# Performance work log

Measured on AMD Instinct MI355X. Metric: run time of the kernel, lower is better.

The kernel has to match this reference:

```python
import jax, jax.numpy as jnp
import numpy as np

B, S, D = 2, 2048, 1024
H, KS, VS = 16, 64, 64

def setup_inputs() -> dict:
    key = jax.random.key(0)
    ks = jax.random.split(key, 11)
    s = 1.0 / np.sqrt(D)
    return {
        "query": jax.random.normal(ks[0], (B, S, D), jnp.float32),
        "key":   jax.random.normal(ks[1], (B, S, D), jnp.float32),
        "value": jax.random.normal(ks[2], (B, S, D), jnp.float32),
        # weights stored [in, out] (transpose of torch Linear)
        "Wq": jax.random.normal(ks[3], (D, H * KS), jnp.float32) * s,
        "bq": jnp.zeros((H * KS,), jnp.float32),
        "Wk": jax.random.normal(ks[4], (D, H * KS), jnp.float32) * s,
        "bk": jnp.zeros((H * KS,), jnp.float32),
        "Wv": jax.random.normal(ks[5], (D, H * VS), jnp.float32) * s,
        "bv": jnp.zeros((H * VS,), jnp.float32),
        "Wo": jax.random.normal(ks[6], (H * VS, D), jnp.float32) * s,
        "bo": jnp.zeros((D,), jnp.float32),
    }

def reference(query, key, value, Wq, bq, Wk, bk, Wv, bv, Wo, bo):
    b = query.shape[0]
    # projections + split heads -> [B, H, S, d]
    Q = (query @ Wq + bq).reshape(b, -1, H, KS).transpose(0, 2, 1, 3)
    K = (key   @ Wk + bk).reshape(b, -1, H, KS).transpose(0, 2, 1, 3)
    V = (value @ Wv + bv).reshape(b, -1, H, VS).transpose(0, 2, 1, 3)
    scores = jnp.einsum('bhqd,bhkd->bhqk', Q, K) / jnp.sqrt(jnp.float32(KS))
    attn = jax.nn.softmax(scores, axis=-1)  # dropout_rate=0.0 -> identity
    ctx = jnp.einsum('bhqk,bhkd->bhqd', attn, V)  # [B,H,S,VS]
    ctx = ctx.transpose(0, 2, 1, 3).reshape(b, attn.shape[-1], H * VS)
    out = ctx @ Wo + bo
    return out, attn
```

## Files before the change

kernel.cpp:

```cpp
#include <hip/hip_runtime.h>
#include <stdint.h>


typedef _Float16 f16;
typedef f16 f16x4 __attribute__((ext_vector_type(4)));
typedef f16 f16x8 __attribute__((ext_vector_type(8)));
typedef float f32x4 __attribute__((ext_vector_type(4)));
typedef uint32_t u32;
typedef u32 u32x4 __attribute__((ext_vector_type(4)));

#define L2E 1.4426950408889634f

__device__ __forceinline__ void gload16(const void* g, void* l) {
    __builtin_amdgcn_global_load_lds((__attribute__((address_space(1))) void*)g,
                                     (__attribute__((address_space(3))) void*)l,
                                     16, 0, 0);
}

__global__ __launch_bounds__(256) void k_cvt(const float* __restrict__ q,
                                             const float* __restrict__ k,
                                             const float* __restrict__ v,
                                             f16* __restrict__ dst)
{
    int z = blockIdx.z;
    const float* s = (z == 0) ? q : (z == 1) ? k : v;
    size_t i = (size_t)blockIdx.x * 256 + threadIdx.x;
    float4 f = ((const float4*)s)[i];
    f16x4 o = {(f16)f.x, (f16)f.y, (f16)f.z, (f16)f.w};
    *(f16x4*)(dst + (size_t)z * 4194304 + i * 4) = o;
}

__global__ __launch_bounds__(256) void k_wtrans(const float* __restrict__ w0,
                                                const float* __restrict__ w1,
                                                const float* __restrict__ w2,
                                                const float* __restrict__ w3,
                                                f16* __restrict__ wt)
{
    __shared__ f16 t[64][72];
    int z = blockIdx.z;
    const float* W = (z == 0) ? w0 : (z == 1) ? w1 : (z == 2) ? w2 : w3;
    f16* outp = wt + (size_t)z * 1048576;
    int tx = blockIdx.x, ty = blockIdx.y, tid = threadIdx.x;
#pragma unroll
    for (int r4 = 0; r4 < 4; r4++) {
        int row = r4 * 16 + (tid >> 4);
        int col = (tid & 15) * 4;
        float4 f = *(const float4*)(W + (size_t)(ty * 64 + row) * 1024 + tx * 64 + col);
        t[col + 0][row] = (f16)f.x; t[col + 1][row] = (f16)f.y;
        t[col + 2][row] = (f16)f.z; t[col + 3][row] = (f16)f.w;
    }
    __syncthreads();
#pragma unroll
    for (int cc = 0; cc < 2; cc++) {
        int c = tid + cc * 256;
        int row = c >> 3, ch = c & 7;
        f16x8 vv;
#pragma unroll
        for (int j = 0; j < 8; j++) vv[j] = t[row][ch * 8 + j];
        *(f16x8*)(outp + (size_t)(tx * 64 + row) * 1024 + ty * 64 + ch * 8) = vv;
    }
}

__global__ __launch_bounds__(256) void k_gemm(const f16* __restrict__ Ab,
                                              const f16* __restrict__ Wtb,
                                              const float* __restrict__ b0,
                                              const float* __restrict__ b1,
                                              const float* __restrict__ b2,
                                              void* __restrict__ o0,
                                              void* __restrict__ o1,
                                              int proj)
{
    __shared__ __align__(16) char As[16384];
    __shared__ __align__(16) char Bs[16384];
    const int tid = threadIdx.x;
    const int wv = tid >> 6, ln = tid & 63, lg = ln >> 4, li = ln & 15;
    const int m0 = blockIdx.y * 128, n0 = blockIdx.x * 128;
    const int wm = (wv >> 1) * 64, wn = (wv & 1) * 64;

    const f16* A; const f16* Bt; const float* bias; int mode;
    if (proj) {
        int z = blockIdx.z;
        A = Ab + (size_t)z * 4194304;
        Bt = Wtb + (size_t)z * 1048576;
        bias = (z == 0) ? b0 : (z == 1) ? b1 : b2;
        mode = (z == 2) ? 1 : 0;
    } else { A = Ab; Bt = Wtb; bias = b0; mode = 2; }

    const char* gA[4]; const char* gB[4];
#pragma unroll
    for (int c = 0; c < 4; c++) {
        int r = (wv * 4 + c) * 8 + (ln >> 3);
        int j = (ln & 7) ^ (r & 7);
        gA[c] = (const char*)A  + (size_t)(m0 + r) * 2048 + j * 16;
        gB[c] = (const char*)Bt + (size_t)(n0 + r) * 2048 + j * 16;
    }

    f32x4 acc[4][4] = {};
    for (int kt = 0; kt < 16; kt++) {
        __syncthreads();
#pragma unroll
        for (int c = 0; c < 4; c++) {
            gload16(gA[c] + kt * 128, As + (wv * 4 + c) * 1024);
            gload16(gB[c] + kt * 128, Bs + (wv * 4 + c) * 1024);
        }
        __syncthreads();
#pragma unroll
        for (int kk = 0; kk < 2; kk++) {
            f16x8 af[4], bf[4];
#pragma unroll
            for (int mi = 0; mi < 4; mi++) {
                int row = wm + mi * 16 + li;
                af[mi] = *(const f16x8*)(As + row * 128 + (((kk * 4 + lg) ^ (row & 7)) * 16));
            }
#pragma unroll
            for (int ni = 0; ni < 4; ni++) {
                int row = wn + ni * 16 + li;
                bf[ni] = *(const f16x8*)(Bs + row * 128 + (((kk * 4 + lg) ^ (row & 7)) * 16));
            }
#pragma unroll
            for (int mi = 0; mi < 4; mi++)
#pragma unroll
                for (int ni = 0; ni < 4; ni++)
                    acc[mi][ni] = __builtin_amdgcn_mfma_f32_16x16x32_f16(af[mi], bf[ni], acc[mi][ni], 0, 0, 0);
        }
    }

    float bvs[4];
#pragma unroll
    for (int ni = 0; ni < 4; ni++) bvs[ni] = bias[n0 + wn + ni * 16 + li];

    if (mode == 2) {
        float* O = (float*)o0;
#pragma unroll
        for (int mi = 0; mi < 4; mi++)
#pragma unroll
            for (int ni = 0; ni < 4; ni++) {
                int n = n0 + wn + ni * 16 + li;
#pragma unroll
                for (int r = 0; r < 4; r++) {
                    int m = m0 + wm + mi * 16 + lg * 4 + r;
                    O[(size_t)m * 1024 + n] = acc[mi][ni][r] + bvs[ni];
                }
            }
    } else if (mode == 0) {
        f16* O = (f16*)o0 + (size_t)blockIdx.z * 4194304;
#pragma unroll
        for (int mi = 0; mi < 4; mi++)
#pragma unroll
            for (int ni = 0; ni < 4; ni++) {
                int n = n0 + wn + ni * 16 + li;
                int h = n >> 6, d = n & 63;
#pragma unroll
                for (int r = 0; r < 4; r++) {
                    int m = m0 + wm + mi * 16 + lg * 4 + r;
                    int b = m >> 11, s = m & 2047;
                    O[(((size_t)b * 16 + h) * 2048 + s) * 64 + d] = (f16)(acc[mi][ni][r] + bvs[ni]);
                }
            }
    } else {
        f16* O = (f16*)o1;
#pragma unroll
        for (int mi = 0; mi < 4; mi++)
#pragma unroll
            for (int ni = 0; ni < 4; ni++) {
                int n = n0 + wn + ni * 16 + li;
                int h = n >> 6, d = n & 63;
                int mb = m0 + wm + mi * 16 + lg * 4;
                int b = mb >> 11, s = mb & 2047;
                f16x4 pk;
#pragma unroll
                for (int r = 0; r < 4; r++) pk[r] = (f16)(acc[mi][ni][r] + bvs[ni]);
                *(f16x4*)(O + (((size_t)b * 16 + h) * 64 + d) * 2048 + s) = pk;
            }
    }
}

__global__ __launch_bounds__(256) void k_attn(const f16* __restrict__ Qb,
                                              const f16* __restrict__ Kb,
                                              const f16* __restrict__ Vt,
                                              float* __restrict__ attn,
                                              f16* __restrict__ ctx)
{
    __shared__ __align__(16) char Ks[8192];
    __shared__ __align__(16) char Vs[8192];
    __shared__ __align__(16) char Ps[4][2048];
    const int tid = threadIdx.x, wv = tid >> 6, ln = tid & 63, lg = ln >> 4, li = ln & 15;
    const int bh = blockIdx.y;
    const int q0 = blockIdx.x * 64 + wv * 16;

    const f16* qrow = Qb + ((size_t)bh * 2048 + q0 + li) * 64 + lg * 8;
    f16x8 aq0 = *(const f16x8*)(qrow);
    f16x8 aq1 = *(const f16x8*)(qrow + 32);
#pragma unroll
    for (int j = 0; j < 8; j++) {
        aq0[j] = (f16)((float)aq0[j] * 0.125f);
        aq1[j] = (f16)((float)aq1[j] * 0.125f);
    }

    const int r0 = tid >> 3, j0 = tid & 7;
    const int r1 = (tid + 256) >> 3, j1 = (tid + 256) & 7;
    const int sw0 = r0 * 128 + ((j0 ^ (r0 & 7)) * 16);
    const int sw1 = r1 * 128 + ((j1 ^ (r1 & 7)) * 16);
    const char* KbB = (const char*)Kb + (size_t)bh * 2048 * 128;
    const char* VtB = (const char*)Vt + (size_t)bh * 64 * 4096;

    float l_ = 0.0f;
    {
        u32x4 sk0 = *(const u32x4*)(KbB + (size_t)r0 * 128 + j0 * 16);
        u32x4 sk1 = *(const u32x4*)(KbB + (size_t)r1 * 128 + j1 * 16);
        for (int kt = 0; kt < 32; kt++) {
            __syncthreads();
            *(u32x4*)(Ks + sw0) = sk0;
            *(u32x4*)(Ks + sw1) = sk1;
            __syncthreads();
            if (kt + 1 < 32) {
                sk0 = *(const u32x4*)(KbB + (size_t)((kt + 1) * 64 + r0) * 128 + j0 * 16);
                sk1 = *(const u32x4*)(KbB + (size_t)((kt + 1) * 64 + r1) * 128 + j1 * 16);
            }
#pragma unroll
            for (int cf = 0; cf < 4; cf++) {
                int row = cf * 16 + li;
                f16x8 ak0 = *(const f16x8*)(Ks + row * 128 + ((lg ^ (row & 7)) * 16));
                f16x8 ak1 = *(const f16x8*)(Ks + row * 128 + (((4 + lg) ^ (row & 7)) * 16));
                f32x4 z = {0.f, 0.f, 0.f, 0.f};
                z = __builtin_amdgcn_mfma_f32_16x16x32_f16(ak0, aq0, z, 0, 0, 0);
                z = __builtin_amdgcn_mfma_f32_16x16x32_f16(ak1, aq1, z, 0, 0, 0);
                l_ += exp2f(z[0] * L2E) + exp2f(z[1] * L2E)
                    + exp2f(z[2] * L2E) + exp2f(z[3] * L2E);
            }
        }
    }
    l_ += __shfl_xor(l_, 16);
    l_ += __shfl_xor(l_, 32);
    const float inv_l = 1.0f / l_;
    float* aRow = attn + ((size_t)bh * 2048 + q0 + li) * 2048;

    f32x4 cacc[4] = {};
    u32x4 sk[2], sv[2];
    sk[0] = *(const u32x4*)(KbB + (size_t)r0 * 128 + j0 * 16);
    sk[1] = *(const u32x4*)(KbB + (size_t)r1 * 128 + j1 * 16);
    sv[0] = *(const u32x4*)(VtB + (size_t)r0 * 4096 + j0 * 16);
    sv[1] = *(const u32x4*)(VtB + (size_t)r1 * 4096 + j1 * 16);
    for (int kt = 0; kt < 32; kt++) {
        __syncthreads();
        *(u32x4*)(Ks + sw0) = sk[0];
        *(u32x4*)(Ks + sw1) = sk[1];
        *(u32x4*)(Vs + sw0) = sv[0];
        *(u32x4*)(Vs + sw1) = sv[1];
        __syncthreads();
        if (kt + 1 < 32) {
            sk[0] = *(const u32x4*)(KbB + (size_t)((kt + 1) * 64 + r0) * 128 + j0 * 16);
            sk[1] = *(const u32x4*)(KbB + (size_t)((kt + 1) * 64 + r1) * 128 + j1 * 16);
            sv[0] = *(const u32x4*)(VtB + (size_t)r0 * 4096 + (kt + 1) * 128 + j0 * 16);
            sv[1] = *(const u32x4*)(VtB + (size_t)r1 * 4096 + (kt + 1) * 128 + j1 * 16);
        }
        char* Pw = Ps[wv];
#pragma unroll
        for (int cf = 0; cf < 4; cf++) {
            int row = cf * 16 + li;
            f16x8 ak0 = *(const f16x8*)(Ks + row * 128 + ((lg ^ (row & 7)) * 16));
            f16x8 ak1 = *(const f16x8*)(Ks + row * 128 + (((4 + lg) ^ (row & 7)) * 16));
            f32x4 z = {0.f, 0.f, 0.f, 0.f};
            z = __builtin_amdgcn_mfma_f32_16x16x32_f16(ak0, aq0, z, 0, 0, 0);
            z = __builtin_amdgcn_mfma_f32_16x16x32_f16(ak1, aq1, z, 0, 0, 0);
            float p0 = exp2f(z[0] * L2E) * inv_l;
            float p1 = exp2f(z[1] * L2E) * inv_l;
            float p2 = exp2f(z[2] * L2E) * inv_l;
            float p3 = exp2f(z[3] * L2E) * inv_l;
            f32x4 fv = {p0, p1, p2, p3};
            __builtin_nontemporal_store(fv, (f32x4*)(aRow + kt * 64 + cf * 16 + lg * 4));
            f16x4 pk = {(f16)p0, (f16)p1, (f16)p2, (f16)p3};
            int c = cf * 2 + (lg >> 1);
            *(f16x4*)(Pw + li * 128 + ((c ^ (li & 7)) * 16) + (lg & 1) * 8) = pk;
        }
#pragma unroll
        for (int s2 = 0; s2 < 2; s2++) {
            f16x8 bp = *(const f16x8*)(Pw + li * 128 + (((s2 * 4 + lg) ^ (li & 7)) * 16));
#pragma unroll
            for (int df = 0; df < 4; df++) {
                int rowv = df * 16 + li;
                f16x8 av = *(const f16x8*)(Vs + rowv * 128 + (((s2 * 4 + lg) ^ (rowv & 7)) * 16));
                cacc[df] = __builtin_amdgcn_mfma_f32_16x16x32_f16(av, bp, cacc[df], 0, 0, 0);
            }
        }
    }
    const int b = bh >> 4, h = bh & 15;
#pragma unroll
    for (int df = 0; df < 4; df++) {
        f16x4 pk;
#pragma unroll
        for (int r = 0; r < 4; r++) pk[r] = (f16)cacc[df][r];
        size_t mrow = (size_t)b * 2048 + q0 + li;
        size_t n = (size_t)h * 64 + df * 16 + lg * 4;
        *(f16x4*)(ctx + mrow * 1024 + n) = pk;
    }
}

extern "C" void kernel_launch(void* const* d_in, const int* in_sizes, int n_in,
                              void* d_out, int out_size, void* d_ws, size_t ws_size,
                              hipStream_t stream)
{
    const float* q  = (const float*)d_in[0];
    const float* k  = (const float*)d_in[1];
    const float* v  = (const float*)d_in[2];
    const float* Wq = (const float*)d_in[3];
    const float* bq = (const float*)d_in[4];
    const float* Wk = (const float*)d_in[5];
    const float* bk = (const float*)d_in[6];
    const float* Wv = (const float*)d_in[7];
    const float* bv = (const float*)d_in[8];
    const float* Wo = (const float*)d_in[9];
    const float* bo = (const float*)d_in[10];

    f16* W = (f16*)d_ws;
    float* out = (float*)d_out;
    float* attn = out + 4194304;

    f16* X   = W;
    f16* Wt  = W + 12582912;
    f16* QKb = W + 16777216;
    f16* Vt  = W + 25165824;
    f16* ctx = W + 29360128;

    k_cvt<<<dim3(4096, 1, 3), 256, 0, stream>>>(q, k, v, X);
    k_wtrans<<<dim3(16, 16, 4), 256, 0, stream>>>(Wq, Wk, Wv, Wo, Wt);
    k_gemm<<<dim3(8, 32, 3), 256, 0, stream>>>(X, Wt, bq, bk, bv, QKb, Vt, 1);
    k_attn<<<dim3(32, 32), 256, 0, stream>>>(QKb, QKb + 4194304, Vt, attn, ctx);
    k_gemm<<<dim3(8, 32, 1), 256, 0, stream>>>(ctx, Wt + 3145728, bo, bo, bo, out, nullptr, 0);
}
```

Measured before the change: 288.5 us.

## Restructure attention kernel: 32 queries per wave, direct global K/V loads, no LDS staging

The attention kernel now gives each wave two 16-row query fragments (128 queries per block), so every K/V fragment loaded is reused across twice as many queries. K and V are read straight from global memory into registers, with software double-buffering in the normalizer pass, replacing the shared-memory staging and its block-wide barriers. Block ids are remapped so each group of 8 consecutive blocks covers 8 different batch-heads, and launch bounds request 2 blocks per CU. The aim is to cut barrier stalls and redundant K/V traffic. In exchange, register pressure rises and global loads become less coalesced, since they are fetched in MFMA fragment layout.

After: 336.8 us. +16.8%, slower.

```diff
diff --git a/kernel.cpp b/kernel.cpp
--- a/kernel.cpp
+++ b/kernel.cpp
@@ -175,125 +175,151 @@
     }
 }
 
-__global__ __launch_bounds__(256) void k_attn(const f16* __restrict__ Qb,
-                                              const f16* __restrict__ Kb,
-                                              const f16* __restrict__ Vt,
-                                              float* __restrict__ attn,
-                                              f16* __restrict__ ctx)
-{
-    __shared__ __align__(16) char Ks[8192];
-    __shared__ __align__(16) char Vs[8192];
-    __shared__ __align__(16) char Ps[4][2048];
+__global__ __launch_bounds__(256, 2) void k_attn(const f16* __restrict__ Qb,
+                                                 const f16* __restrict__ Kb,
+                                                 const f16* __restrict__ Vt,
+                                                 float* __restrict__ attn,
+                                                 f16* __restrict__ ctx)
+{
+    __shared__ __align__(16) char Ps[16384];
     const int tid = threadIdx.x, wv = tid >> 6, ln = tid & 63, lg = ln >> 4, li = ln & 15;
-    const int bh = blockIdx.y;
-    const int q0 = blockIdx.x * 64 + wv * 16;
-
-    const f16* qrow = Qb + ((size_t)bh * 2048 + q0 + li) * 64 + lg * 8;
-    f16x8 aq0 = *(const f16x8*)(qrow);
-    f16x8 aq1 = *(const f16x8*)(qrow + 32);
-#pragma unroll
-    for (int j = 0; j < 8; j++) {
-        aq0[j] = (f16)((float)aq0[j] * 0.125f);
-        aq1[j] = (f16)((float)aq1[j] * 0.125f);
-    }
-
-    const int r0 = tid >> 3, j0 = tid & 7;
-    const int r1 = (tid + 256) >> 3, j1 = (tid + 256) & 7;
-    const int sw0 = r0 * 128 + ((j0 ^ (r0 & 7)) * 16);
-    const int sw1 = r1 * 128 + ((j1 ^ (r1 & 7)) * 16);
-    const char* KbB = (const char*)Kb + (size_t)bh * 2048 * 128;
-    const char* VtB = (const char*)Vt + (size_t)bh * 64 * 4096;
-
-    float l_ = 0.0f;
+    const int bid = blockIdx.x;
+    const int kk = bid >> 3;
+    const int bh = (bid & 7) * 4 + (kk >> 4);
+    const int q0 = (kk & 15) * 128 + wv * 32;
+
+    const char* KbB = (const char*)Kb + (size_t)bh * 262144;
+    const char* VtB = (const char*)Vt + (size_t)bh * 262144;
+
+    f16x8 aq[2][2];
+#pragma unroll
+    for (int qf = 0; qf < 2; qf++) {
+        const f16* qrow = Qb + ((size_t)bh * 2048 + q0 + qf * 16 + li) * 64 + lg * 8;
+        aq[qf][0] = *(const f16x8*)(qrow);
+        aq[qf][1] = *(const f16x8*)(qrow + 32);
+#pragma unroll
+        for (int j = 0; j < 8; j++) {
+            aq[qf][0][j] = (f16)((float)aq[qf][0][j] * 0.125f);
+            aq[qf][1][j] = (f16)((float)aq[qf][1][j] * 0.125f);
+        }
+    }
+
+#define LOADK(buf, kt) do { \
+    _Pragma("unroll") for (int cf = 0; cf < 4; cf++) { \
+        const char* kr = KbB + (size_t)((kt) * 64 + cf * 16 + li) * 128 + lg * 16; \
+        buf[cf][0] = *(const f16x8*)kr; \
+        buf[cf][1] = *(const f16x8*)(kr + 64); \
+    } } while (0)
+
+#define QKT(zz, buf) do { \
+    _Pragma("unroll") for (int cf = 0; cf < 4; cf++) { \
+        f32x4 z0 = {0.f,0.f,0.f,0.f}, z1 = {0.f,0.f,0.f,0.f}; \
+        z0 = __builtin_amdgcn_mfma_f32_16x16x32_f16(buf[cf][0], aq[0][0], z0, 0, 0, 0); \
+        z0 = __builtin_amdgcn_mfma_f32_16x16x32_f16(buf[cf][1], aq[0][1], z0, 0, 0, 0); \
+        z1 = __builtin_amdgcn_mfma_f32_16x16x32_f16(buf[cf][0], aq[1][0], z1, 0, 0, 0); \
+        z1 = __builtin_amdgcn_mfma_f32_16x16x32_f16(buf[cf][1], aq[1][1], z1, 0, 0, 0); \
+        zz[0][cf] = z0; zz[1][cf] = z1; \
+    } } while (0)
+
+    float l_[2] = {0.f, 0.f};
     {
-        u32x4 sk0 = *(const u32x4*)(KbB + (size_t)r0 * 128 + j0 * 16);
-        u32x4 sk1 = *(const u32x4*)(KbB + (size_t)r1 * 128 + j1 * 16);
-        for (int kt = 0; kt < 32; kt++) {
-            __syncthreads();
-            *(u32x4*)(Ks + sw0) = sk0;
-            *(u32x4*)(Ks + sw1) = sk1;
-            __syncthreads();
-            if (kt + 1 < 32) {
-                sk0 = *(const u32x4*)(KbB + (size_t)((kt + 1) * 64 + r0) * 128 + j0 * 16);
-                sk1 = *(const u32x4*)(KbB + (size_t)((kt + 1) * 64 + r1) * 128 + j1 * 16);
-            }
+        f16x8 ka[4][2], kb[4][2];
+        LOADK(ka, 0);
+        for (int kt2 = 0; kt2 < 16; kt2++) {
+            LOADK(kb, 2 * kt2 + 1);
+            {
+                f32x4 zz[2][4];
+                QKT(zz, ka);
+#pragma unroll
+                for (int qf = 0; qf < 2; qf++)
+#pragma unroll
+                    for (int cf = 0; cf < 4; cf++)
+                        l_[qf] += exp2f(zz[qf][cf][0] * L2E) + exp2f(zz[qf][cf][1] * L2E)
+                                + exp2f(zz[qf][cf][2] * L2E) + exp2f(zz[qf][cf][3] * L2E);
+            }
+            if (kt2 + 1 < 16) LOADK(ka, 2 * kt2 + 2);
+            {
+                f32x4 zz[2][4];
+                QKT(zz, kb);
+#pragma unroll
+                for (int qf = 0; qf < 2; qf++)
+#pragma unroll
+                    for (int cf = 0; cf < 4; cf++)
+                        l_[qf] += exp2f(zz[qf][cf][0] * L2E) + exp2f(zz[qf][cf][1] * L2E)
+                                + exp2f(zz[qf][cf][2] * L2E) + exp2f(zz[qf][cf][3] * L2E);
+            }
+        }
+    }
+    float inv_l[2];
+#pragma unroll
+    for (int qf = 0; qf < 2; qf++) {
+        l_[qf] += __shfl_xor(l_[qf], 16);
+        l_[qf] += __shfl_xor(l_[qf], 32);
+        inv_l[qf] = 1.0f / l_[qf];
+    }
+    float* aR[2];
+    aR[0] = attn + ((size_t)bh * 2048 + q0 + li) * 2048;
+    aR[1] = aR[0] + 16 * 2048;
+    char* Pw0 = Ps + (wv * 2) * 2048;
+    char* Pw1 = Ps + (wv * 2 + 1) * 2048;
+
+    f32x4 cacc[2][4] = {};
+#pragma unroll 2
+    for (int kt = 0; kt < 32; kt++) {
+        f16x8 kf[4][2];
+        LOADK(kf, kt);
+        f32x4 zz[2][4];
+        QKT(zz, kf);
+        f16x8 vf[4][2];
+#pragma unroll
+        for (int df = 0; df < 4; df++) {
+            const char* vr = VtB + (size_t)(df * 16 + li) * 4096 + kt * 128 + lg * 16;
+            vf[df][0] = *(const f16x8*)vr;
+            vf[df][1] = *(const f16x8*)(vr + 64);
+        }
+#pragma unroll
+        for (int qf = 0; qf < 2; qf++) {
+            char* Pw = qf ? Pw1 : Pw0;
 #pragma unroll
             for (int cf = 0; cf < 4; cf++) {
-                int row = cf * 16 + li;
-                f16x8 ak0 = *(const f16x8*)(Ks + row * 128 + ((lg ^ (row & 7)) * 16));
-                f16x8 ak1 = *(const f16x8*)(Ks + row * 128 + (((4 + lg) ^ (row & 7)) * 16));
-                f32x4 z = {0.f, 0.f, 0.f, 0.f};
-                z = __builtin_amdgcn_mfma_f32_16x16x32_f16(ak0, aq0, z, 0, 0, 0);
-                z = __builtin_amdgcn_mfma_f32_16x16x32_f16(ak1, aq1, z, 0, 0, 0);
-                l_ += exp2f(z[0] * L2E) + exp2f(z[1] * L2E)
-                    + exp2f(z[2] * L2E) + exp2f(z[3] * L2E);
-            }
-        }
-    }
-    l_ += __shfl_xor(l_, 16);
-    l_ += __shfl_xor(l_, 32);
-    const float inv_l = 1.0f / l_;
-    float* aRow = attn + ((size_t)bh * 2048 + q0 + li) * 2048;
-
-    f32x4 cacc[4] = {};
-    u32x4 sk[2], sv[2];
-    sk[0] = *(const u32x4*)(KbB + (size_t)r0 * 128 + j0 * 16);
-    sk[1] = *(const u32x4*)(KbB + (size_t)r1 * 128 + j1 * 16);
-    sv[0] = *(const u32x4*)(VtB + (size_t)r0 * 4096 + j0 * 16);
-    sv[1] = *(const u32x4*)(VtB + (size_t)r1 * 4096 + j1 * 16);
-    for (int kt = 0; kt < 32; kt++) {
-        __syncthreads();
-        *(u32x4*)(Ks + sw0) = sk[0];
-        *(u32x4*)(Ks + sw1) = sk[1];
-        *(u32x4*)(Vs + sw0) = sv[0];
-        *(u32x4*)(Vs + sw1) = sv[1];
-        __syncthreads();
-        if (kt + 1 < 32) {
-            sk[0] = *(const u32x4*)(KbB + (size_t)((kt + 1) * 64 + r0) * 128 + j0 * 16);
-            sk[1] = *(const u32x4*)(KbB + (size_t)((kt + 1) * 64 + r1) * 128 + j1 * 16);
-            sv[0] = *(const u32x4*)(VtB + (size_t)r0 * 4096 + (kt + 1) * 128 + j0 * 16);
-            sv[1] = *(const u32x4*)(VtB + (size_t)r1 * 4096 + (kt + 1) * 128 + j1 * 16);
-        }
-        char* Pw = Ps[wv];
-#pragma unroll
-        for (int cf = 0; cf < 4; cf++) {
-            int row = cf * 16 + li;
-            f16x8 ak0 = *(const f16x8*)(Ks + row * 128 + ((lg ^ (row & 7)) * 16));
-            f16x8 ak1 = *(const f16x8*)(Ks + row * 128 + (((4 + lg) ^ (row & 7)) * 16));
-            f32x4 z = {0.f, 0.f, 0.f, 0.f};
-            z = __builtin_amdgcn_mfma_f32_16x16x32_f16(ak0, aq0, z, 0, 0, 0);
-            z = __builtin_amdgcn_mfma_f32_16x16x32_f16(ak1, aq1, z, 0, 0, 0);
-            float p0 = exp2f(z[0] * L2E) * inv_l;
-            float p1 = exp2f(z[1] * L2E) * inv_l;
-            float p2 = exp2f(z[2] * L2E) * inv_l;
-            float p3 = exp2f(z[3] * L2E) * inv_l;
-            f32x4 fv = {p0, p1, p2, p3};
-            __builtin_nontemporal_store(fv, (f32x4*)(aRow + kt * 64 + cf * 16 + lg * 4));
-            f16x4 pk = {(f16)p0, (f16)p1, (f16)p2, (f16)p3};
-            int c = cf * 2 + (lg >> 1);
-            *(f16x4*)(Pw + li * 128 + ((c ^ (li & 7)) * 16) + (lg & 1) * 8) = pk;
-        }
-#pragma unroll
-        for (int s2 = 0; s2 < 2; s2++) {
-            f16x8 bp = *(const f16x8*)(Pw + li * 128 + (((s2 * 4 + lg) ^ (li & 7)) * 16));
-#pragma unroll
-            for (int df = 0; df < 4; df++) {
-                int rowv = df * 16 + li;
-                f16x8 av = *(const f16x8*)(Vs + rowv * 128 + (((s2 * 4 + lg) ^ (rowv & 7)) * 16));
-                cacc[df] = __builtin_amdgcn_mfma_f32_16x16x32_f16(av, bp, cacc[df], 0, 0, 0);
-            }
-        }
-    }
+                float p0 = exp2f(zz[qf][cf][0] * L2E) * inv_l[qf];
+                float p1 = exp2f(zz[qf][cf][1] * L2E) * inv_l[qf];
+                float p2 = exp2f(zz[qf][cf][2] * L2E) * inv_l[qf];
+                float p3 = exp2f(zz[qf][cf][3] * L2E) * inv_l[qf];
+                f32x4 fv = {p0, p1, p2, p3};
+                __builtin_nontemporal_store(fv, (f32x4*)(aR[qf] + kt * 64 + cf * 16 + lg * 4));
+                f16x4 pk = {(f16)p0, (f16)p1, (f16)p2, (f16)p3};
+                int c = cf * 2 + (lg >> 1);
+                *(f16x4*)(Pw + li * 128 + ((c ^ (li & 7)) * 16) + (lg & 1) * 8) = pk;
+            }
+        }
+#pragma unroll
+        for (int qf = 0; qf < 2; qf++) {
+            char* Pw = qf ? Pw1 : Pw0;
+#pragma unroll
+            for (int s2 = 0; s2 < 2; s2++) {
+                f16x8 bp = *(const f16x8*)(Pw + li * 128 + (((s2 * 4 + lg) ^ (li & 7)) * 16));
+#pragma unroll
+                for (int df = 0; df < 4; df++)
+                    cacc[qf][df] = __builtin_amdgcn_mfma_f32_16x16x32_f16(vf[df][s2], bp, cacc[qf][df], 0, 0, 0);
+            }
+        }
+    }
+#undef LOADK
+#undef QKT
+
     const int b = bh >> 4, h = bh & 15;
 #pragma unroll
-    for (int df = 0; df < 4; df++) {
-        f16x4 pk;
-#pragma unroll
-        for (int r = 0; r < 4; r++) pk[r] = (f16)cacc[df][r];
-        size_t mrow = (size_t)b * 2048 + q0 + li;
-        size_t n = (size_t)h * 64 + df * 16 + lg * 4;
-        *(f16x4*)(ctx + mrow * 1024 + n) = pk;
-    }
+    for (int qf = 0; qf < 2; qf++)
+#pragma unroll
+        for (int df = 0; df < 4; df++) {
+            f16x4 pk;
+#pragma unroll
+            for (int r = 0; r < 4; r++) pk[r] = (f16)cacc[qf][df][r];
+            size_t mrow = (size_t)b * 2048 + q0 + qf * 16 + li;
+            size_t n = (size_t)h * 64 + df * 16 + lg * 4;
+            *(f16x4*)(ctx + mrow * 1024 + n) = pk;
+        }
 }
 
 extern "C" void kernel_launch(void* const* d_in, const int* in_sizes, int n_in,
@@ -325,6 +351,6 @@
     k_cvt<<<dim3(4096, 1, 3), 256, 0, stream>>>(q, k, v, X);
     k_wtrans<<<dim3(16, 16, 4), 256, 0, stream>>>(Wq, Wk, Wv, Wo, Wt);
     k_gemm<<<dim3(8, 32, 3), 256, 0, stream>>>(X, Wt, bq, bk, bv, QKb, Vt, 1);
-    k_attn<<<dim3(32, 32), 256, 0, stream>>>(QKb, QKb + 4194304, Vt, attn, ctx);
+    k_attn<<<dim3(512), 256, 0, stream>>>(QKb, QKb + 4194304, Vt, attn, ctx);
     k_gemm<<<dim3(8, 32, 1), 256, 0, stream>>>(ctx, Wt + 3145728, bo, bo, bo, out, nullptr, 0);
 }
```

## Restructure attention kernel: direct V loads, larger K tiles, remapped grid

Applied to the files above, without the earlier changes.

The attention kernel now reads V fragments straight from global memory into registers instead of staging them through shared memory. The first pass, which only sums the softmax denominator, uses 128-row K tiles with split accumulators, halving its barrier count. The grid is flattened so that blocks are ordered across heads to spread head data across XCDs/L2, and a launch-bounds occupancy hint is added. It also splits the QK MFMA and the exp/store phases to expose more ILP. The trade-off is more uncoalesced global loads for V, against less LDS use and fewer syncs.

Result: faster. 275.2 us (-4.6%).

```diff
diff --git a/kernel.cpp b/kernel.cpp
--- a/kernel.cpp
+++ b/kernel.cpp
@@ -175,18 +175,22 @@
     }
 }
 
-__global__ __launch_bounds__(256) void k_attn(const f16* __restrict__ Qb,
-                                              const f16* __restrict__ Kb,
-                                              const f16* __restrict__ Vt,
-                                              float* __restrict__ attn,
-                                              f16* __restrict__ ctx)
-{
-    __shared__ __align__(16) char Ks[8192];
-    __shared__ __align__(16) char Vs[8192];
+__global__ __launch_bounds__(256, 3) void k_attn(const f16* __restrict__ Qb,
+                                                 const f16* __restrict__ Kb,
+                                                 const f16* __restrict__ Vt,
+                                                 float* __restrict__ attn,
+                                                 f16* __restrict__ ctx)
+{
+    __shared__ __align__(16) char Ks[16384];
     __shared__ __align__(16) char Ps[4][2048];
     const int tid = threadIdx.x, wv = tid >> 6, ln = tid & 63, lg = ln >> 4, li = ln & 15;
-    const int bh = blockIdx.y;
-    const int q0 = blockIdx.x * 64 + wv * 16;
+    const int bid = blockIdx.x;
+    const int kk = bid >> 3;
+    const int bh = (bid & 7) * 4 + (kk >> 5);
+    const int q0 = (kk & 31) * 64 + wv * 16;
+
+    const char* KbB = (const char*)Kb + (size_t)bh * 262144;
+    const char* VtB = (const char*)Vt + (size_t)bh * 262144;
 
     const f16* qrow = Qb + ((size_t)bh * 2048 + q0 + li) * 64 + lg * 8;
     f16x8 aq0 = *(const f16x8*)(qrow);
@@ -197,64 +201,74 @@
         aq1[j] = (f16)((float)aq1[j] * 0.125f);
     }
 
-    const int r0 = tid >> 3, j0 = tid & 7;
-    const int r1 = (tid + 256) >> 3, j1 = (tid + 256) & 7;
-    const int sw0 = r0 * 128 + ((j0 ^ (r0 & 7)) * 16);
-    const int sw1 = r1 * 128 + ((j1 ^ (r1 & 7)) * 16);
-    const char* KbB = (const char*)Kb + (size_t)bh * 2048 * 128;
-    const char* VtB = (const char*)Vt + (size_t)bh * 64 * 4096;
-
-    float l_ = 0.0f;
+    float lacc[4] = {0.f, 0.f, 0.f, 0.f};
     {
-        u32x4 sk0 = *(const u32x4*)(KbB + (size_t)r0 * 128 + j0 * 16);
-        u32x4 sk1 = *(const u32x4*)(KbB + (size_t)r1 * 128 + j1 * 16);
-        for (int kt = 0; kt < 32; kt++) {
+        int rr[4], swp[4];
+        const char* gp[4];
+#pragma unroll
+        for (int t = 0; t < 4; t++) {
+            int c = tid + t * 256;
+            int r = c >> 3, j = c & 7;
+            rr[t] = r;
+            swp[t] = r * 128 + ((j ^ (r & 7)) * 16);
+            gp[t] = KbB + (size_t)r * 128 + j * 16;
+        }
+        u32x4 s[4];
+#pragma unroll
+        for (int t = 0; t < 4; t++) s[t] = *(const u32x4*)(gp[t]);
+        for (int kt = 0; kt < 16; kt++) {
             __syncthreads();
-            *(u32x4*)(Ks + sw0) = sk0;
-            *(u32x4*)(Ks + sw1) = sk1;
+#pragma unroll
+            for (int t = 0; t < 4; t++) *(u32x4*)(Ks + swp[t]) = s[t];
             __syncthreads();
-            if (kt + 1 < 32) {
-                sk0 = *(const u32x4*)(KbB + (size_t)((kt + 1) * 64 + r0) * 128 + j0 * 16);
-                sk1 = *(const u32x4*)(KbB + (size_t)((kt + 1) * 64 + r1) * 128 + j1 * 16);
-            }
-#pragma unroll
-            for (int cf = 0; cf < 4; cf++) {
+            if (kt + 1 < 16) {
+#pragma unroll
+                for (int t = 0; t < 4; t++) s[t] = *(const u32x4*)(gp[t] + (size_t)(kt + 1) * 16384);
+            }
+#pragma unroll
+            for (int cf = 0; cf < 8; cf++) {
                 int row = cf * 16 + li;
                 f16x8 ak0 = *(const f16x8*)(Ks + row * 128 + ((lg ^ (row & 7)) * 16));
                 f16x8 ak1 = *(const f16x8*)(Ks + row * 128 + (((4 + lg) ^ (row & 7)) * 16));
                 f32x4 z = {0.f, 0.f, 0.f, 0.f};
                 z = __builtin_amdgcn_mfma_f32_16x16x32_f16(ak0, aq0, z, 0, 0, 0);
                 z = __builtin_amdgcn_mfma_f32_16x16x32_f16(ak1, aq1, z, 0, 0, 0);
-                l_ += exp2f(z[0] * L2E) + exp2f(z[1] * L2E)
-                    + exp2f(z[2] * L2E) + exp2f(z[3] * L2E);
-            }
-        }
-    }
+                lacc[cf & 3] += exp2f(z[0] * L2E) + exp2f(z[1] * L2E)
+                              + exp2f(z[2] * L2E) + exp2f(z[3] * L2E);
+            }
+        }
+    }
+    float l_ = (lacc[0] + lacc[1]) + (lacc[2] + lacc[3]);
     l_ += __shfl_xor(l_, 16);
     l_ += __shfl_xor(l_, 32);
     const float inv_l = 1.0f / l_;
     float* aRow = attn + ((size_t)bh * 2048 + q0 + li) * 2048;
+    char* Pw = Ps[wv];
 
     f32x4 cacc[4] = {};
-    u32x4 sk[2], sv[2];
-    sk[0] = *(const u32x4*)(KbB + (size_t)r0 * 128 + j0 * 16);
-    sk[1] = *(const u32x4*)(KbB + (size_t)r1 * 128 + j1 * 16);
-    sv[0] = *(const u32x4*)(VtB + (size_t)r0 * 4096 + j0 * 16);
-    sv[1] = *(const u32x4*)(VtB + (size_t)r1 * 4096 + j1 * 16);
+    const int r0 = tid >> 3, j0 = tid & 7;
+    const int r1 = (tid + 256) >> 3, j1 = (tid + 256) & 7;
+    const int sw0 = r0 * 128 + ((j0 ^ (r0 & 7)) * 16);
+    const int sw1 = r1 * 128 + ((j1 ^ (r1 & 7)) * 16);
+    u32x4 sk0 = *(const u32x4*)(KbB + (size_t)r0 * 128 + j0 * 16);
+    u32x4 sk1 = *(const u32x4*)(KbB + (size_t)r1 * 128 + j1 * 16);
     for (int kt = 0; kt < 32; kt++) {
         __syncthreads();
-        *(u32x4*)(Ks + sw0) = sk[0];
-        *(u32x4*)(Ks + sw1) = sk[1];
-        *(u32x4*)(Vs + sw0) = sv[0];
-        *(u32x4*)(Vs + sw1) = sv[1];
+        *(u32x4*)(Ks + sw0) = sk0;
+        *(u32x4*)(Ks + sw1) = sk1;
         __syncthreads();
         if (kt + 1 < 32) {
-            sk[0] = *(const u32x4*)(KbB + (size_t)((kt + 1) * 64 + r0) * 128 + j0 * 16);
-            sk[1] = *(const u32x4*)(KbB + (size_t)((kt + 1) * 64 + r1) * 128 + j1 * 16);
-            sv[0] = *(const u32x4*)(VtB + (size_t)r0 * 4096 + (kt + 1) * 128 + j0 * 16);
-            sv[1] = *(const u32x4*)(VtB + (size_t)r1 * 4096 + (kt + 1) * 128 + j1 * 16);
-        }
-        char* Pw = Ps[wv];
+            sk0 = *(const u32x4*)(KbB + (size_t)((kt + 1) * 64 + r0) * 128 + j0 * 16);
+            sk1 = *(const u32x4*)(KbB + (size_t)((kt + 1) * 64 + r1) * 128 + j1 * 16);
+        }
+        f16x8 vf[4][2];
+#pragma unroll
+        for (int df = 0; df < 4; df++) {
+            const char* vr = VtB + (size_t)(df * 16 + li) * 4096 + kt * 128 + lg * 16;
+            vf[df][0] = *(const f16x8*)vr;
+            vf[df][1] = *(const f16x8*)(vr + 64);
+        }
+        f32x4 zz[4];
 #pragma unroll
         for (int cf = 0; cf < 4; cf++) {
             int row = cf * 16 + li;
@@ -263,10 +277,14 @@
             f32x4 z = {0.f, 0.f, 0.f, 0.f};
             z = __builtin_amdgcn_mfma_f32_16x16x32_f16(ak0, aq0, z, 0, 0, 0);
             z = __builtin_amdgcn_mfma_f32_16x16x32_f16(ak1, aq1, z, 0, 0, 0);
-            float p0 = exp2f(z[0] * L2E) * inv_l;
-            float p1 = exp2f(z[1] * L2E) * inv_l;
-            float p2 = exp2f(z[2] * L2E) * inv_l;
-            float p3 = exp2f(z[3] * L2E) * inv_l;
+            zz[cf] = z;
+        }
+#pragma unroll
+        for (int cf = 0; cf < 4; cf++) {
+            float p0 = exp2f(zz[cf][0] * L2E) * inv_l;
+            float p1 = exp2f(zz[cf][1] * L2E) * inv_l;
+            float p2 = exp2f(zz[cf][2] * L2E) * inv_l;
+            float p3 = exp2f(zz[cf][3] * L2E) * inv_l;
             f32x4 fv = {p0, p1, p2, p3};
             __builtin_nontemporal_store(fv, (f32x4*)(aRow + kt * 64 + cf * 16 + lg * 4));
             f16x4 pk = {(f16)p0, (f16)p1, (f16)p2, (f16)p3};
@@ -277,13 +295,11 @@
         for (int s2 = 0; s2 < 2; s2++) {
             f16x8 bp = *(const f16x8*)(Pw + li * 128 + (((s2 * 4 + lg) ^ (li & 7)) * 16));
 #pragma unroll
-            for (int df = 0; df < 4; df++) {
-                int rowv = df * 16 + li;
-                f16x8 av = *(const f16x8*)(Vs + rowv * 128 + (((s2 * 4 + lg) ^ (rowv & 7)) * 16));
-                cacc[df] = __builtin_amdgcn_mfma_f32_16x16x32_f16(av, bp, cacc[df], 0, 0, 0);
-            }
-        }
-    }
+            for (int df = 0; df < 4; df++)
+                cacc[df] = __builtin_amdgcn_mfma_f32_16x16x32_f16(vf[df][s2], bp, cacc[df], 0, 0, 0);
+        }
+    }
+
     const int b = bh >> 4, h = bh & 15;
 #pragma unroll
     for (int df = 0; df < 4; df++) {
@@ -325,6 +341,6 @@
     k_cvt<<<dim3(4096, 1, 3), 256, 0, stream>>>(q, k, v, X);
     k_wtrans<<<dim3(16, 16, 4), 256, 0, stream>>>(Wq, Wk, Wv, Wo, Wt);
     k_gemm<<<dim3(8, 32, 3), 256, 0, stream>>>(X, Wt, bq, bk, bv, QKb, Vt, 1);
-    k_attn<<<dim3(32, 32), 256, 0, stream>>>(QKb, QKb + 4194304, Vt, attn, ctx);
+    k_attn<<<dim3(1024), 256, 0, stream>>>(QKb, QKb + 4194304, Vt, attn, ctx);
     k_gemm<<<dim3(8, 32, 1), 256, 0, stream>>>(ctx, Wt + 3145728, bo, bo, bo, out, nullptr, 0);
 }
```
